# Kernel tuning notes

Hardware: AMD Instinct MI355X
Metric: run time of the kernel (lower is better)

Reference implementation:

```python
import jax, jax.numpy as jnp
import numpy as np

N = 100000    # nodes
E = 1600000   # edges (avg degree 16)
IN = 128      # input feature dim
D = 32        # per-head hidden dim
H = 4         # heads for hidden layers
C = 16        # num_classes (final per-head dim)
NEG = 0.2     # leaky_relu negative slope


def setup_inputs() -> dict:
    key = jax.random.key(0)
    ks = jax.random.split(key, 14)
    s = jnp.float32(0.05)
    f32 = jnp.float32
    inp = {
        "inputs": jax.random.normal(ks[0], (N, IN), f32),
        "src": jax.random.randint(ks[1], (E,), 0, N),
        "dst": jax.random.randint(ks[2], (E,), 0, N),
        # layer 0: IN -> (H, D), no residual
        "W0": jax.random.normal(ks[3], (IN, H * D), f32) * s,
        "al0": jax.random.normal(ks[4], (H, D), f32) * s,
        "ar0": jax.random.normal(ks[5], (H, D), f32) * s,
        # layer 1: H*D -> (H, D), identity residual (dims match)
        "W1": jax.random.normal(ks[6], (H * D, H * D), f32) * s,
        "al1": jax.random.normal(ks[7], (H, D), f32) * s,
        "ar1": jax.random.normal(ks[8], (H, D), f32) * s,
        # final layer: H*D -> (1, C), linear residual projection
        "W2": jax.random.normal(ks[9], (H * D, 1 * C), f32) * s,
        "al2": jax.random.normal(ks[10], (1, C), f32) * s,
        "ar2": jax.random.normal(ks[11], (1, C), f32) * s,
        "resW2": jax.random.normal(ks[12], (H * D, 1 * C), f32) * s,
    }
    return inp


def gat_conv(h, W, al, ar, src, dst, n_heads, out_dim, res=None, act=None):
    # h: (N, F_in) -> out: (N, n_heads, out_dim)
    feat = (h @ W).reshape(N, n_heads, out_dim)            # (N,H,D)
    el = jnp.sum(feat * al, axis=-1)                       # (N,H)
    er = jnp.sum(feat * ar, axis=-1)                       # (N,H)
    e = jax.nn.leaky_relu(el[src] + er[dst], NEG)          # (E,H)
    # softmax over incoming edges per destination node
    emax = jax.ops.segment_max(e, dst, num_segments=N)     # (N,H)
    ex = jnp.exp(e - emax[dst])                            # (E,H)
    den = jax.ops.segment_sum(ex, dst, num_segments=N)     # (N,H)
    alpha = ex / den[dst]                                  # (E,H)
    msg = feat[src] * alpha[:, :, None]                    # (E,H,D) -- dominant traffic
    out = jax.ops.segment_sum(msg, dst, num_segments=N)    # (N,H,D)
    if res is not None:
        out = out + res
    if act is not None:
        out = act(out)
    return out


def reference(inputs, src, dst, W0, al0, ar0, W1, al1, ar1, W2, al2, ar2, resW2):
    # hidden layer 0 (no residual), GATConv activation = elu, then flatten + relu
    h = gat_conv(inputs, W0, al0, ar0, src, dst, H, D, res=None, act=jax.nn.elu)
    h = jax.nn.relu(h.reshape(N, H * D))
    # hidden layer 1, identity residual (in == H*D)
    res1 = h.reshape(N, H, D)
    h = gat_conv(h, W1, al1, ar1, src, dst, H, D, res=res1, act=jax.nn.elu)
    h = jax.nn.relu(h.reshape(N, H * D))
    # output layer: 1 head, linear residual projection, no activation, mean over heads
    res2 = (h @ resW2).reshape(N, 1, C)
    out = gat_conv(h, W2, al2, ar2, src, dst, 1, C, res=res2, act=None)
    return out.mean(axis=1)                                # (N, C)
```

## Files before the change

kernel.cpp:

```cpp
#include <hip/hip_runtime.h>

#define N_NODES 100000
#define N_EDGES 1600000
#define IN_F    128
#define NEG_SLOPE 0.2f
#define NBUCK   512
#define PCHUNK  4096

typedef __attribute__((ext_vector_type(8))) short bf16x8;
typedef __attribute__((ext_vector_type(4))) float f32x4;

__device__ __forceinline__ float bf2f(unsigned short u) {
    return __uint_as_float(((unsigned int)u) << 16);
}

__device__ __forceinline__ unsigned short f2bf(float f) {
    unsigned int u = __float_as_uint(f);
    u += 0x7FFFu + ((u >> 16) & 1u);
    return (unsigned short)(u >> 16);
}

__global__ __launch_bounds__(256) void pack_all(const float* __restrict__ W0,
                                                const float* __restrict__ W1,
                                                const float* __restrict__ W2,
                                                const float* __restrict__ rW2,
                                                unsigned short* __restrict__ W0p,
                                                unsigned short* __restrict__ W1p,
                                                unsigned short* __restrict__ W2p) {
    int gid = blockIdx.x * 256 + threadIdx.x;
    const float* W;
    unsigned short* Wp;
    int idx, ncols;
    if (gid < 16384)      { W = W0; Wp = W0p; idx = gid;          ncols = 128; }
    else if (gid < 32768) { W = W1; Wp = W1p; idx = gid - 16384;  ncols = 128; }
    else                  { W = W2; Wp = W2p; idx = gid - 32768;  ncols = 32;  }
    int j  = idx & 7;
    int l  = (idx >> 3) & 63;
    int kt = (idx >> 9) & 3;
    int nt = idx >> 11;
    int k  = kt * 32 + (l >> 4) * 8 + j;
    int n  = nt * 16 + (l & 15);
    float v;
    if (ncols == 128) v = W[k * 128 + n];
    else              v = (n < 16) ? W[k * 16 + n] : rW2[k * 16 + (n - 16)];
    Wp[idx] = f2bf(v);
}

__global__ __launch_bounds__(256) void gemm128_mfma_f32(const float* __restrict__ A,
                                                        const unsigned short* __restrict__ Wp,
                                                        const float* __restrict__ al,
                                                        const float* __restrict__ ar,
                                                        unsigned short* __restrict__ featb,
                                                        float* __restrict__ el,
                                                        float* __restrict__ er,
                                                        int nrows) {
    const int t    = threadIdx.x;
    const int wv   = t >> 6;
    const int lane = t & 63;
    const int q    = lane >> 4;
    const int m    = lane & 15;
    const int rb   = blockIdx.x * 64 + wv * 16;
    const int arow = rb + m;
    const bool rok = arow < nrows;
    const float* Ar = A + (size_t)arow * IN_F;

    f32x4 acc[8];
#pragma unroll
    for (int nt = 0; nt < 8; ++nt) acc[nt] = (f32x4){0.f, 0.f, 0.f, 0.f};

#pragma unroll
    for (int kt = 0; kt < 4; ++kt) {
        bf16x8 afr = (bf16x8){0, 0, 0, 0, 0, 0, 0, 0};
        if (rok) {
            float4 v0 = *(const float4*)(Ar + kt * 32 + q * 8);
            float4 v1 = *(const float4*)(Ar + kt * 32 + q * 8 + 4);
            afr[0] = (short)f2bf(v0.x); afr[1] = (short)f2bf(v0.y);
            afr[2] = (short)f2bf(v0.z); afr[3] = (short)f2bf(v0.w);
            afr[4] = (short)f2bf(v1.x); afr[5] = (short)f2bf(v1.y);
            afr[6] = (short)f2bf(v1.z); afr[7] = (short)f2bf(v1.w);
        }
#pragma unroll
        for (int nt = 0; nt < 8; ++nt) {
            bf16x8 bfr = *(const bf16x8*)(Wp + ((size_t)(nt * 4 + kt) * 64 + lane) * 8);
            acc[nt] = __builtin_amdgcn_mfma_f32_16x16x32_bf16(afr, bfr, acc[nt], 0, 0, 0);
        }
    }

    float pel[16], per[16];
#pragma unroll
    for (int i = 0; i < 16; ++i) { pel[i] = 0.f; per[i] = 0.f; }

#pragma unroll
    for (int nt = 0; nt < 8; ++nt) {
        const int col = nt * 16 + m;
        const float alv = al[col];
        const float arv = ar[col];
        const int h = nt >> 1;
#pragma unroll
        for (int reg = 0; reg < 4; ++reg) {
            int row = rb + q * 4 + reg;
            float a = acc[nt][reg];
            if (row < nrows) featb[(size_t)row * 128 + col] = f2bf(a);
            pel[reg * 4 + h] += a * alv;
            per[reg * 4 + h] += a * arv;
        }
    }
#pragma unroll
    for (int s = 8; s > 0; s >>= 1) {
#pragma unroll
        for (int i = 0; i < 16; ++i) {
            pel[i] += __shfl_down(pel[i], s);
            per[i] += __shfl_down(per[i], s);
        }
    }
    if (m == 0) {
#pragma unroll
        for (int reg = 0; reg < 4; ++reg) {
            int row = rb + q * 4 + reg;
            if (row < nrows) {
#pragma unroll
                for (int h = 0; h < 4; ++h) {
                    el[row * 4 + h] = pel[reg * 4 + h];
                    er[row * 4 + h] = per[reg * 4 + h];
                }
            }
        }
    }
}

__global__ __launch_bounds__(256) void gemm128_mfma_bf16(const unsigned short* __restrict__ Ab,
                                                         const unsigned short* __restrict__ Wp,
                                                         const float* __restrict__ al,
                                                         const float* __restrict__ ar,
                                                         unsigned short* __restrict__ featb,
                                                         float* __restrict__ el,
                                                         float* __restrict__ er,
                                                         int nrows) {
    const int t    = threadIdx.x;
    const int wv   = t >> 6;
    const int lane = t & 63;
    const int q    = lane >> 4;
    const int m    = lane & 15;
    const int rb   = blockIdx.x * 64 + wv * 16;
    const int arow = rb + m;
    const bool rok = arow < nrows;
    const unsigned short* Ar = Ab + (size_t)arow * IN_F;

    f32x4 acc[8];
#pragma unroll
    for (int nt = 0; nt < 8; ++nt) acc[nt] = (f32x4){0.f, 0.f, 0.f, 0.f};

#pragma unroll
    for (int kt = 0; kt < 4; ++kt) {
        bf16x8 afr = (bf16x8){0, 0, 0, 0, 0, 0, 0, 0};
        if (rok) afr = *(const bf16x8*)(Ar + kt * 32 + q * 8);
#pragma unroll
        for (int nt = 0; nt < 8; ++nt) {
            bf16x8 bfr = *(const bf16x8*)(Wp + ((size_t)(nt * 4 + kt) * 64 + lane) * 8);
            acc[nt] = __builtin_amdgcn_mfma_f32_16x16x32_bf16(afr, bfr, acc[nt], 0, 0, 0);
        }
    }

    float pel[16], per[16];
#pragma unroll
    for (int i = 0; i < 16; ++i) { pel[i] = 0.f; per[i] = 0.f; }

#pragma unroll
    for (int nt = 0; nt < 8; ++nt) {
        const int col = nt * 16 + m;
        const float alv = al[col];
        const float arv = ar[col];
        const int h = nt >> 1;
#pragma unroll
        for (int reg = 0; reg < 4; ++reg) {
            int row = rb + q * 4 + reg;
            float a = acc[nt][reg];
            if (row < nrows) featb[(size_t)row * 128 + col] = f2bf(a);
            pel[reg * 4 + h] += a * alv;
            per[reg * 4 + h] += a * arv;
        }
    }
#pragma unroll
    for (int s = 8; s > 0; s >>= 1) {
#pragma unroll
        for (int i = 0; i < 16; ++i) {
            pel[i] += __shfl_down(pel[i], s);
            per[i] += __shfl_down(per[i], s);
        }
    }
    if (m == 0) {
#pragma unroll
        for (int reg = 0; reg < 4; ++reg) {
            int row = rb + q * 4 + reg;
            if (row < nrows) {
#pragma unroll
                for (int h = 0; h < 4; ++h) {
                    el[row * 4 + h] = pel[reg * 4 + h];
                    er[row * 4 + h] = per[reg * 4 + h];
                }
            }
        }
    }
}

__global__ __launch_bounds__(256) void gemm16_mfma(const unsigned short* __restrict__ Ab,
                                                   const unsigned short* __restrict__ Wp,
                                                   const float* __restrict__ al,
                                                   const float* __restrict__ ar,
                                                   unsigned short* __restrict__ feat2b,
                                                   float* __restrict__ res2,
                                                   float* __restrict__ el,
                                                   float* __restrict__ er,
                                                   int nrows) {
    const int t    = threadIdx.x;
    const int wv   = t >> 6;
    const int lane = t & 63;
    const int q    = lane >> 4;
    const int m    = lane & 15;
    const int rb   = blockIdx.x * 64 + wv * 16;
    const int arow = rb + m;
    const bool rok = arow < nrows;
    const unsigned short* Ar = Ab + (size_t)arow * IN_F;

    f32x4 acc0 = (f32x4){0.f, 0.f, 0.f, 0.f};
    f32x4 acc1 = (f32x4){0.f, 0.f, 0.f, 0.f};

#pragma unroll
    for (int kt = 0; kt < 4; ++kt) {
        bf16x8 afr = (bf16x8){0, 0, 0, 0, 0, 0, 0, 0};
        if (rok) afr = *(const bf16x8*)(Ar + kt * 32 + q * 8);
        bf16x8 b0 = *(const bf16x8*)(Wp + ((size_t)(0 * 4 + kt) * 64 + lane) * 8);
        bf16x8 b1 = *(const bf16x8*)(Wp + ((size_t)(1 * 4 + kt) * 64 + lane) * 8);
        acc0 = __builtin_amdgcn_mfma_f32_16x16x32_bf16(afr, b0, acc0, 0, 0, 0);
        acc1 = __builtin_amdgcn_mfma_f32_16x16x32_bf16(afr, b1, acc1, 0, 0, 0);
    }

    float pel[4], per[4];
    const float alv = al[m];
    const float arv = ar[m];
#pragma unroll
    for (int reg = 0; reg < 4; ++reg) {
        int row = rb + q * 4 + reg;
        float a = acc0[reg];
        if (row < nrows) {
            feat2b[(size_t)row * 16 + m] = f2bf(a);
            res2[(size_t)row * 16 + m]   = acc1[reg];
        }
        pel[reg] = a * alv;
        per[reg] = a * arv;
    }
#pragma unroll
    for (int s = 8; s > 0; s >>= 1) {
#pragma unroll
        for (int reg = 0; reg < 4; ++reg) {
            pel[reg] += __shfl_down(pel[reg], s);
            per[reg] += __shfl_down(per[reg], s);
        }
    }
    if (m == 0) {
#pragma unroll
        for (int reg = 0; reg < 4; ++reg) {
            int row = rb + q * 4 + reg;
            if (row < nrows) { el[row] = pel[reg]; er[row] = per[reg]; }
        }
    }
}

__global__ __launch_bounds__(256) void bucket_count_k(const int* __restrict__ dst,
                                                      int* __restrict__ bcount, int nE) {
    __shared__ int hist[NBUCK];
    const int t = threadIdx.x;
    hist[t] = 0; hist[t + 256] = 0;
    __syncthreads();
    const int start = blockIdx.x * PCHUNK;
#pragma unroll
    for (int j = 0; j < PCHUNK / 256; ++j) {
        int e = start + j * 256 + t;
        if (e < nE) atomicAdd(&hist[dst[e] >> 8], 1);
    }
    __syncthreads();
    if (hist[t])       atomicAdd(&bcount[t],       hist[t]);
    if (hist[t + 256]) atomicAdd(&bcount[t + 256], hist[t + 256]);
}

__global__ __launch_bounds__(NBUCK) void scan512(const int* __restrict__ bcount,
                                                 int* __restrict__ bbase,
                                                 int* __restrict__ bcursor) {
    __shared__ int s[NBUCK];
    const int t = threadIdx.x;
    int v = bcount[t];
    s[t] = v;
    __syncthreads();
#pragma unroll
    for (int off = 1; off < NBUCK; off <<= 1) {
        int x = (t >= off) ? s[t - off] : 0;
        __syncthreads();
        s[t] += x;
        __syncthreads();
    }
    int excl = s[t] - v;
    bbase[t]   = excl;
    bcursor[t] = excl;
}

__global__ __launch_bounds__(512) void partition_k(const int* __restrict__ src,
                                                   const int* __restrict__ dst,
                                                   int* __restrict__ bcursor,
                                                   unsigned int* __restrict__ pe, int nE) {
    __shared__ int hist[NBUCK];
    __shared__ int lstart[NBUCK];
    __shared__ int gbase[NBUCK];
    __shared__ int curB[NBUCK];
    __shared__ unsigned int reorder[PCHUNK];

    const int t = threadIdx.x;
    const int start = blockIdx.x * PCHUNK;
    const int m = min(PCHUNK, nE - start);

    hist[t] = 0;
    __syncthreads();

#pragma unroll
    for (int j = 0; j < PCHUNK / 512; ++j) {
        int e = start + j * 512 + t;
        if (e < nE) atomicAdd(&hist[dst[e] >> 8], 1);
    }
    __syncthreads();
    const int cnt = hist[t];

    __shared__ int s[NBUCK];
    s[t] = cnt;
    __syncthreads();
#pragma unroll
    for (int off = 1; off < NBUCK; off <<= 1) {
        int x = (t >= off) ? s[t - off] : 0;
        __syncthreads();
        s[t] += x;
        __syncthreads();
    }
    lstart[t] = s[t] - cnt;
    curB[t]   = s[t] - cnt;
    gbase[t] = cnt ? atomicAdd(&bcursor[t], cnt) : 0;
    __syncthreads();

#pragma unroll
    for (int j = 0; j < PCHUNK / 512; ++j) {
        int e = start + j * 512 + t;
        if (e < nE) {
            int d = dst[e];
            int pos = atomicAdd(&curB[d >> 8], 1);
            reorder[pos] = ((unsigned)src[e] << 8) | ((unsigned)d & 255u);
        }
    }
    __syncthreads();

    for (int i = t; i < m; i += 512) {
        unsigned int ed = reorder[i];
        int lo = 0, hi = NBUCK - 1;
        while (lo < hi) {
            int mid = (lo + hi + 1) >> 1;
            if (lstart[mid] <= i) lo = mid; else hi = mid - 1;
        }
        pe[gbase[lo] + (i - lstart[lo])] = ed;
    }
}

__global__ __launch_bounds__(256) void bucket_finalize(const unsigned int* __restrict__ pe,
                                                       const int* __restrict__ bbase,
                                                       int* __restrict__ rowptr,
                                                       int* __restrict__ deg,
                                                       int* __restrict__ sorted_src,
                                                       int nE) {
    __shared__ int deg_l[256];
    __shared__ int s[256];
    __shared__ int cur[256];

    const int b  = blockIdx.x;
    const int t  = threadIdx.x;
    const int base = bbase[b];
    const int endE = (b + 1 < NBUCK) ? bbase[b + 1] : nE;
    const int cnt  = endE - base;
    const int n    = b * 256 + t;

    deg_l[t] = 0;
    __syncthreads();
    for (int i = t; i < cnt; i += 256)
        atomicAdd(&deg_l[pe[base + i] & 255u], 1);
    __syncthreads();

    const int dv = deg_l[t];
    s[t] = dv;
    __syncthreads();
#pragma unroll
    for (int off = 1; off < 256; off <<= 1) {
        int x = (t >= off) ? s[t - off] : 0;
        __syncthreads();
        s[t] += x;
        __syncthreads();
    }
    const int off_l = s[t] - dv;
    if (n < N_NODES) {
        rowptr[n] = base + off_l;
        deg[n]    = dv;
    }
    cur[t] = off_l;
    __syncthreads();

    for (int i = t; i < cnt; i += 256) {
        unsigned int ed = pe[base + i];
        int pos = atomicAdd(&cur[ed & 255u], 1);
        sorted_src[base + pos] = (int)(ed >> 8);
    }
}

__global__ __launch_bounds__(256) void gat_agg128(const int* __restrict__ rowptr,
                                                  const int* __restrict__ deg,
                                                  const int* __restrict__ sorted_src,
                                                  const float* __restrict__ el,
                                                  const float* __restrict__ er,
                                                  const unsigned short* __restrict__ featb,
                                                  const unsigned short* __restrict__ resb,
                                                  unsigned short* __restrict__ outb) {
    __shared__ int   sS[4][64];
    __shared__ float sW[4][64][4];

    const int wv   = threadIdx.x >> 6;
    const int lane = threadIdx.x & 63;
    const int nd   = blockIdx.x * 4 + wv;

    const int dg = deg[nd];
    const int r0 = rowptr[nd];
    const int h  = lane >> 4;
    const float4 er4 = *(const float4*)(er + nd * 4);

    float den = 0.f;
    float ax = 0.f, ay = 0.f;

    for (int base = 0; base < dg; base += 64) {
        int m = dg - base; if (m > 64) m = 64;
        if (lane < m) {
            int s = sorted_src[r0 + base + lane];
            sS[wv][lane] = s;
            float4 e4 = *(const float4*)(el + s * 4);
            float4 w;
            float v;
            v = e4.x + er4.x; v = v > 0.f ? v : NEG_SLOPE * v; w.x = __expf(v);
            v = e4.y + er4.y; v = v > 0.f ? v : NEG_SLOPE * v; w.y = __expf(v);
            v = e4.z + er4.z; v = v > 0.f ? v : NEG_SLOPE * v; w.z = __expf(v);
            v = e4.w + er4.w; v = v > 0.f ? v : NEG_SLOPE * v; w.w = __expf(v);
            *(float4*)(&sW[wv][lane][0]) = w;
        }
        for (int i = 0; i < m; ++i) {
            int s   = sS[wv][i];
            float w = sW[wv][i][h];
            den += w;
            ushort2 u = *(const ushort2*)(featb + (size_t)s * 128 + lane * 2);
            ax += w * bf2f(u.x);
            ay += w * bf2f(u.y);
        }
    }

    float scale = den > 0.f ? 1.f / den : 0.f;
    float ox = ax * scale, oy = ay * scale;
    size_t o0 = (size_t)nd * 128 + lane * 2;
    if (resb) {
        ushort2 rv = *(const ushort2*)(resb + o0);
        ox += bf2f(rv.x);
        oy += bf2f(rv.y);
    }
    ox = fmaxf(ox, 0.f);
    oy = fmaxf(oy, 0.f);
    ushort2 ou;
    ou.x = f2bf(ox);
    ou.y = f2bf(oy);
    *(ushort2*)(outb + o0) = ou;
}

__global__ __launch_bounds__(256) void gat_agg16(const int* __restrict__ rowptr,
                                                 const int* __restrict__ deg,
                                                 const int* __restrict__ sorted_src,
                                                 const float* __restrict__ el,
                                                 const float* __restrict__ er,
                                                 const unsigned short* __restrict__ feat2b,
                                                 const float* __restrict__ res,
                                                 float* __restrict__ out) {
    __shared__ int   sS[4][64];
    __shared__ float sW[4][64];

    const int wv   = threadIdx.x >> 6;
    const int lane = threadIdx.x & 63;
    const int nd   = blockIdx.x * 4 + wv;
    const int g    = lane >> 3;
    const int f2   = (lane & 7) * 2;

    const int dg = deg[nd];
    const int r0 = rowptr[nd];
    const float erd = er[nd];

    float ax = 0.f, ay = 0.f, den = 0.f;

    for (int base = 0; base < dg; base += 64) {
        int m = dg - base; if (m > 64) m = 64;
        if (lane < m) {
            int s = sorted_src[r0 + base + lane];
            sS[wv][lane] = s;
            float v = el[s] + erd;
            v = v > 0.f ? v : NEG_SLOPE * v;
            sW[wv][lane] = __expf(v);
        }
        for (int i = g; i < m; i += 8) {
            int s   = sS[wv][i];
            float w = sW[wv][i];
            den += w;
            ushort2 u = *(const ushort2*)(feat2b + (size_t)s * 16 + f2);
            ax += w * bf2f(u.x);
            ay += w * bf2f(u.y);
        }
    }

    ax += __shfl_down(ax, 32); ay += __shfl_down(ay, 32); den += __shfl_down(den, 32);
    ax += __shfl_down(ax, 16); ay += __shfl_down(ay, 16); den += __shfl_down(den, 16);
    ax += __shfl_down(ax, 8);  ay += __shfl_down(ay, 8);  den += __shfl_down(den, 8);

    if (lane < 8) {
        float scale = den > 0.f ? 1.f / den : 0.f;
        size_t o0 = (size_t)nd * 16 + f2;
        float2 o;
        o.x = ax * scale + res[o0];
        o.y = ay * scale + res[o0 + 1];
        *(float2*)(out + o0) = o;
    }
}

extern "C" void kernel_launch(void* const* d_in, const int* in_sizes, int n_in,
                              void* d_out, int out_size, void* d_ws, size_t ws_size,
                              hipStream_t stream) {
    const float* inputs = (const float*)d_in[0];
    const int*   src    = (const int*)d_in[1];
    const int*   dst    = (const int*)d_in[2];
    const float* W0     = (const float*)d_in[3];
    const float* al0    = (const float*)d_in[4];
    const float* ar0    = (const float*)d_in[5];
    const float* W1     = (const float*)d_in[6];
    const float* al1    = (const float*)d_in[7];
    const float* ar1    = (const float*)d_in[8];
    const float* W2     = (const float*)d_in[9];
    const float* al2    = (const float*)d_in[10];
    const float* ar2    = (const float*)d_in[11];
    const float* resW2  = (const float*)d_in[12];
    float* out = (float*)d_out;

    const size_t NF = (size_t)N_NODES * 128;
    float* ws   = (float*)d_ws;
    float* el   = ws;
    float* er   = el + (size_t)N_NODES * 4;
    float* res2 = er + (size_t)N_NODES * 4;
    unsigned short* hbufb  = (unsigned short*)(res2 + (size_t)N_NODES * 16);
    unsigned short* featb  = hbufb + NF;
    unsigned short* feat2b = featb + NF;
    unsigned short* W0p    = feat2b + (size_t)N_NODES * 16;
    unsigned short* W1p    = W0p + 16384;
    unsigned short* W2p    = W1p + 16384;
    int* iws = (int*)(W2p + 8192);
    unsigned int* pe = (unsigned int*)iws;
    int* deg         = iws + N_EDGES;
    int* rowptr      = deg + N_NODES;
    int* sorted_src  = rowptr + N_NODES;
    int* bcount      = sorted_src + N_EDGES;
    int* bbase       = bcount + NBUCK;
    int* bcursor     = bbase + NBUCK;

    dim3 blk(256);
    int gemmGrid = (N_NODES + 63) / 64;
    int pGrid    = (N_EDGES + PCHUNK - 1) / PCHUNK;
    int bGrid    = (N_NODES + 255) / 256;
    int aggGrid  = N_NODES / 4;

    hipMemsetAsync(bcount, 0, NBUCK * sizeof(int), stream);
    bucket_count_k<<<pGrid, blk, 0, stream>>>(dst, bcount, N_EDGES);
    scan512<<<1, NBUCK, 0, stream>>>(bcount, bbase, bcursor);
    partition_k<<<pGrid, dim3(512), 0, stream>>>(src, dst, bcursor, pe, N_EDGES);
    bucket_finalize<<<bGrid, blk, 0, stream>>>(pe, bbase, rowptr, deg, sorted_src, N_EDGES);
    pack_all<<<160, blk, 0, stream>>>(W0, W1, W2, resW2, W0p, W1p, W2p);

    gemm128_mfma_f32<<<gemmGrid, blk, 0, stream>>>(inputs, W0p, al0, ar0, featb,
                                                   el, er, N_NODES);
    gat_agg128<<<aggGrid, blk, 0, stream>>>(rowptr, deg, sorted_src, el, er, featb,
                                            nullptr, hbufb);

    gemm128_mfma_bf16<<<gemmGrid, blk, 0, stream>>>(hbufb, W1p, al1, ar1, featb,
                                                    el, er, N_NODES);
    gat_agg128<<<aggGrid, blk, 0, stream>>>(rowptr, deg, sorted_src, el, er, featb,
                                            hbufb, hbufb);

    gemm16_mfma<<<gemmGrid, blk, 0, stream>>>(hbufb, W2p, al2, ar2, feat2b, res2,
                                              el, er, N_NODES);
    gat_agg16<<<aggGrid, blk, 0, stream>>>(rowptr, deg, sorted_src, el, er, feat2b,
                                           res2, out);
}
```

Before: 412.7 us.

## Horizontally fuse edge partitioning with layer-0 GEMM and bucket counting with weight packing

Merges the bucket-count kernel with weight packing, and the edge-partition kernel with the layer-0 feature GEMM, into single launches whose blocks branch on blockIdx. This cuts launch count and lets independent preprocessing and GEMM work overlap on the device. The partition step moves to 256 threads and records each slot's bucket in shared memory, replacing the per-element binary search. Nontemporal loads and stores are added on streaming accesses. The fused partition/GEMM kernel reserves about 34 KB of shared memory for every block, including GEMM blocks that do not use it, which may lower their occupancy.

```diff
diff --git a/kernel.cpp b/kernel.cpp
--- a/kernel.cpp
+++ b/kernel.cpp
@@ -6,9 +6,14 @@
 #define NEG_SLOPE 0.2f
 #define NBUCK   512
 #define PCHUNK  4096
+#define PGRID   391
+#define GEMMGRID 1563
+#define PACKGRID 160
 
 typedef __attribute__((ext_vector_type(8))) short bf16x8;
 typedef __attribute__((ext_vector_type(4))) float f32x4;
+typedef __attribute__((ext_vector_type(2))) float f32x2;
+typedef __attribute__((ext_vector_type(2))) unsigned short u16x2;
 
 __device__ __forceinline__ float bf2f(unsigned short u) {
     return __uint_as_float(((unsigned int)u) << 16);
@@ -20,111 +25,263 @@
     return (unsigned short)(u >> 16);
 }
 
-__global__ __launch_bounds__(256) void pack_all(const float* __restrict__ W0,
-                                                const float* __restrict__ W1,
-                                                const float* __restrict__ W2,
-                                                const float* __restrict__ rW2,
-                                                unsigned short* __restrict__ W0p,
-                                                unsigned short* __restrict__ W1p,
-                                                unsigned short* __restrict__ W2p) {
-    int gid = blockIdx.x * 256 + threadIdx.x;
-    const float* W;
-    unsigned short* Wp;
-    int idx, ncols;
-    if (gid < 16384)      { W = W0; Wp = W0p; idx = gid;          ncols = 128; }
-    else if (gid < 32768) { W = W1; Wp = W1p; idx = gid - 16384;  ncols = 128; }
-    else                  { W = W2; Wp = W2p; idx = gid - 32768;  ncols = 32;  }
-    int j  = idx & 7;
-    int l  = (idx >> 3) & 63;
-    int kt = (idx >> 9) & 3;
-    int nt = idx >> 11;
-    int k  = kt * 32 + (l >> 4) * 8 + j;
-    int n  = nt * 16 + (l & 15);
-    float v;
-    if (ncols == 128) v = W[k * 128 + n];
-    else              v = (n < 16) ? W[k * 16 + n] : rW2[k * 16 + (n - 16)];
-    Wp[idx] = f2bf(v);
-}
-
-__global__ __launch_bounds__(256) void gemm128_mfma_f32(const float* __restrict__ A,
-                                                        const unsigned short* __restrict__ Wp,
-                                                        const float* __restrict__ al,
-                                                        const float* __restrict__ ar,
-                                                        unsigned short* __restrict__ featb,
-                                                        float* __restrict__ el,
-                                                        float* __restrict__ er,
-                                                        int nrows) {
-    const int t    = threadIdx.x;
-    const int wv   = t >> 6;
-    const int lane = t & 63;
-    const int q    = lane >> 4;
-    const int m    = lane & 15;
-    const int rb   = blockIdx.x * 64 + wv * 16;
-    const int arow = rb + m;
-    const bool rok = arow < nrows;
-    const float* Ar = A + (size_t)arow * IN_F;
-
-    f32x4 acc[8];
-#pragma unroll
-    for (int nt = 0; nt < 8; ++nt) acc[nt] = (f32x4){0.f, 0.f, 0.f, 0.f};
-
-#pragma unroll
-    for (int kt = 0; kt < 4; ++kt) {
-        bf16x8 afr = (bf16x8){0, 0, 0, 0, 0, 0, 0, 0};
-        if (rok) {
-            float4 v0 = *(const float4*)(Ar + kt * 32 + q * 8);
-            float4 v1 = *(const float4*)(Ar + kt * 32 + q * 8 + 4);
-            afr[0] = (short)f2bf(v0.x); afr[1] = (short)f2bf(v0.y);
-            afr[2] = (short)f2bf(v0.z); afr[3] = (short)f2bf(v0.w);
-            afr[4] = (short)f2bf(v1.x); afr[5] = (short)f2bf(v1.y);
-            afr[6] = (short)f2bf(v1.z); afr[7] = (short)f2bf(v1.w);
-        }
+__global__ __launch_bounds__(256) void count_pack(const int* __restrict__ dst,
+                                                  int* __restrict__ bcount, int nE,
+                                                  const float* __restrict__ W0,
+                                                  const float* __restrict__ W1,
+                                                  const float* __restrict__ W2,
+                                                  const float* __restrict__ rW2,
+                                                  unsigned short* __restrict__ W0p,
+                                                  unsigned short* __restrict__ W1p,
+                                                  unsigned short* __restrict__ W2p) {
+    __shared__ int hist[NBUCK];
+    const int t = threadIdx.x;
+    if (blockIdx.x < PGRID) {
+        hist[t] = 0; hist[t + 256] = 0;
+        __syncthreads();
+        const int start = blockIdx.x * PCHUNK;
+#pragma unroll
+        for (int j = 0; j < PCHUNK / 256; ++j) {
+            int e = start + j * 256 + t;
+            if (e < nE) atomicAdd(&hist[__builtin_nontemporal_load(dst + e) >> 8], 1);
+        }
+        __syncthreads();
+        if (hist[t])       atomicAdd(&bcount[t],       hist[t]);
+        if (hist[t + 256]) atomicAdd(&bcount[t + 256], hist[t + 256]);
+    } else {
+        int gid = (blockIdx.x - PGRID) * 256 + t;
+        const float* W;
+        unsigned short* Wp;
+        int idx, ncols;
+        if (gid < 16384)      { W = W0; Wp = W0p; idx = gid;          ncols = 128; }
+        else if (gid < 32768) { W = W1; Wp = W1p; idx = gid - 16384;  ncols = 128; }
+        else                  { W = W2; Wp = W2p; idx = gid - 32768;  ncols = 32;  }
+        int j  = idx & 7;
+        int l  = (idx >> 3) & 63;
+        int kt = (idx >> 9) & 3;
+        int nt = idx >> 11;
+        int k  = kt * 32 + (l >> 4) * 8 + j;
+        int n  = nt * 16 + (l & 15);
+        float v;
+        if (ncols == 128) v = W[k * 128 + n];
+        else              v = (n < 16) ? W[k * 16 + n] : rW2[k * 16 + (n - 16)];
+        Wp[idx] = f2bf(v);
+    }
+}
+
+__global__ __launch_bounds__(NBUCK) void scan512(const int* __restrict__ bcount,
+                                                 int* __restrict__ bbase,
+                                                 int* __restrict__ bcursor) {
+    __shared__ int s[NBUCK];
+    const int t = threadIdx.x;
+    int v = bcount[t];
+    s[t] = v;
+    __syncthreads();
+#pragma unroll
+    for (int off = 1; off < NBUCK; off <<= 1) {
+        int x = (t >= off) ? s[t - off] : 0;
+        __syncthreads();
+        s[t] += x;
+        __syncthreads();
+    }
+    int excl = s[t] - v;
+    bbase[t]   = excl;
+    bcursor[t] = excl;
+}
+
+__global__ __launch_bounds__(256) void part_gemm0(const int* __restrict__ src,
+                                                  const int* __restrict__ dst,
+                                                  int* __restrict__ bcursor,
+                                                  unsigned int* __restrict__ pe, int nE,
+                                                  const float* __restrict__ A,
+                                                  const unsigned short* __restrict__ Wp,
+                                                  const float* __restrict__ al,
+                                                  const float* __restrict__ ar,
+                                                  unsigned short* __restrict__ featb,
+                                                  float* __restrict__ el,
+                                                  float* __restrict__ er,
+                                                  int nrows) {
+    __shared__ int hist[NBUCK];
+    __shared__ int lstart[NBUCK];
+    __shared__ int gbase[NBUCK];
+    __shared__ int curB[NBUCK];
+    __shared__ int s[NBUCK];
+    __shared__ unsigned int  reorder[PCHUNK];
+    __shared__ unsigned short bmem[PCHUNK];
+
+    const int t = threadIdx.x;
+
+    if (blockIdx.x < PGRID) {
+        const int start = blockIdx.x * PCHUNK;
+        const int m = min(PCHUNK, nE - start);
+
+        hist[t] = 0; hist[t + 256] = 0;
+        __syncthreads();
+#pragma unroll
+        for (int j = 0; j < PCHUNK / 256; ++j) {
+            int e = start + j * 256 + t;
+            if (e < nE) atomicAdd(&hist[__builtin_nontemporal_load(dst + e) >> 8], 1);
+        }
+        __syncthreads();
+        const int c0 = hist[t];
+        const int c1 = hist[t + 256];
+        s[t] = c0; s[t + 256] = c1;
+        __syncthreads();
+#pragma unroll
+        for (int off = 1; off <= 256; off <<= 1) {
+            int x0 = (t >= off) ? s[t - off] : 0;
+            int x1 = s[t + 256 - off];
+            __syncthreads();
+            s[t] += x0; s[t + 256] += x1;
+            __syncthreads();
+        }
+        lstart[t]       = s[t] - c0;
+        lstart[t + 256] = s[t + 256] - c1;
+        curB[t]         = s[t] - c0;
+        curB[t + 256]   = s[t + 256] - c1;
+        gbase[t]        = c0 ? atomicAdd(&bcursor[t],       c0) : 0;
+        gbase[t + 256]  = c1 ? atomicAdd(&bcursor[t + 256], c1) : 0;
+        __syncthreads();
+
+#pragma unroll
+        for (int j = 0; j < PCHUNK / 256; ++j) {
+            int e = start + j * 256 + t;
+            if (e < nE) {
+                int d  = __builtin_nontemporal_load(dst + e);
+                int sv = __builtin_nontemporal_load(src + e);
+                int b  = d >> 8;
+                int pos = atomicAdd(&curB[b], 1);
+                reorder[pos] = ((unsigned)sv << 8) | ((unsigned)d & 255u);
+                bmem[pos]    = (unsigned short)b;
+            }
+        }
+        __syncthreads();
+
+        for (int i = t; i < m; i += 256) {
+            int b = bmem[i];
+            __builtin_nontemporal_store(reorder[i], pe + gbase[b] + (i - lstart[b]));
+        }
+    } else {
+        const int bid  = blockIdx.x - PGRID;
+        const int wv   = t >> 6;
+        const int lane = t & 63;
+        const int q    = lane >> 4;
+        const int m    = lane & 15;
+        const int rb   = bid * 64 + wv * 16;
+        const int arow = rb + m;
+        const bool rok = arow < nrows;
+        const float* Ar = A + (size_t)arow * IN_F;
+
+        f32x4 acc[8];
+#pragma unroll
+        for (int nt = 0; nt < 8; ++nt) acc[nt] = (f32x4){0.f, 0.f, 0.f, 0.f};
+
+#pragma unroll
+        for (int kt = 0; kt < 4; ++kt) {
+            bf16x8 afr = (bf16x8){0, 0, 0, 0, 0, 0, 0, 0};
+            if (rok) {
+                f32x4 v0 = __builtin_nontemporal_load((const f32x4*)(Ar + kt * 32 + q * 8));
+                f32x4 v1 = __builtin_nontemporal_load((const f32x4*)(Ar + kt * 32 + q * 8 + 4));
+                afr[0] = (short)f2bf(v0.x); afr[1] = (short)f2bf(v0.y);
+                afr[2] = (short)f2bf(v0.z); afr[3] = (short)f2bf(v0.w);
+                afr[4] = (short)f2bf(v1.x); afr[5] = (short)f2bf(v1.y);
+                afr[6] = (short)f2bf(v1.z); afr[7] = (short)f2bf(v1.w);
+            }
+#pragma unroll
+            for (int nt = 0; nt < 8; ++nt) {
+                bf16x8 bfr = *(const bf16x8*)(Wp + ((size_t)(nt * 4 + kt) * 64 + lane) * 8);
+                acc[nt] = __builtin_amdgcn_mfma_f32_16x16x32_bf16(afr, bfr, acc[nt], 0, 0, 0);
+            }
+        }
+
+        float pel[16], per[16];
+#pragma unroll
+        for (int i = 0; i < 16; ++i) { pel[i] = 0.f; per[i] = 0.f; }
+
 #pragma unroll
         for (int nt = 0; nt < 8; ++nt) {
-            bf16x8 bfr = *(const bf16x8*)(Wp + ((size_t)(nt * 4 + kt) * 64 + lane) * 8);
-            acc[nt] = __builtin_amdgcn_mfma_f32_16x16x32_bf16(afr, bfr, acc[nt], 0, 0, 0);
-        }
-    }
-
-    float pel[16], per[16];
-#pragma unroll
-    for (int i = 0; i < 16; ++i) { pel[i] = 0.f; per[i] = 0.f; }
-
-#pragma unroll
-    for (int nt = 0; nt < 8; ++nt) {
-        const int col = nt * 16 + m;
-        const float alv = al[col];
-        const float arv = ar[col];
-        const int h = nt >> 1;
-#pragma unroll
-        for (int reg = 0; reg < 4; ++reg) {
-            int row = rb + q * 4 + reg;
-            float a = acc[nt][reg];
-            if (row < nrows) featb[(size_t)row * 128 + col] = f2bf(a);
-            pel[reg * 4 + h] += a * alv;
-            per[reg * 4 + h] += a * arv;
-        }
-    }
-#pragma unroll
-    for (int s = 8; s > 0; s >>= 1) {
-#pragma unroll
-        for (int i = 0; i < 16; ++i) {
-            pel[i] += __shfl_down(pel[i], s);
-            per[i] += __shfl_down(per[i], s);
-        }
-    }
-    if (m == 0) {
-#pragma unroll
-        for (int reg = 0; reg < 4; ++reg) {
-            int row = rb + q * 4 + reg;
-            if (row < nrows) {
-#pragma unroll
-                for (int h = 0; h < 4; ++h) {
-                    el[row * 4 + h] = pel[reg * 4 + h];
-                    er[row * 4 + h] = per[reg * 4 + h];
+            const int col = nt * 16 + m;
+            const float alv = al[col];
+            const float arv = ar[col];
+            const int h = nt >> 1;
+#pragma unroll
+            for (int reg = 0; reg < 4; ++reg) {
+                int row = rb + q * 4 + reg;
+                float a = acc[nt][reg];
+                if (row < nrows) featb[(size_t)row * 128 + col] = f2bf(a);
+                pel[reg * 4 + h] += a * alv;
+                per[reg * 4 + h] += a * arv;
+            }
+        }
+#pragma unroll
+        for (int sh = 8; sh > 0; sh >>= 1) {
+#pragma unroll
+            for (int i = 0; i < 16; ++i) {
+                pel[i] += __shfl_down(pel[i], sh);
+                per[i] += __shfl_down(per[i], sh);
+            }
+        }
+        if (m == 0) {
+#pragma unroll
+            for (int reg = 0; reg < 4; ++reg) {
+                int row = rb + q * 4 + reg;
+                if (row < nrows) {
+#pragma unroll
+                    for (int h = 0; h < 4; ++h) {
+                        el[row * 4 + h] = pel[reg * 4 + h];
+                        er[row * 4 + h] = per[reg * 4 + h];
+                    }
                 }
             }
         }
+    }
+}
+
+__global__ __launch_bounds__(256) void bucket_finalize(const unsigned int* __restrict__ pe,
+                                                       const int* __restrict__ bbase,
+                                                       int* __restrict__ rowptr,
+                                                       int* __restrict__ deg,
+                                                       int* __restrict__ sorted_src,
+                                                       int nE) {
+    __shared__ int deg_l[256];
+    __shared__ int s[256];
+    __shared__ int cur[256];
+
+    const int b  = blockIdx.x;
+    const int t  = threadIdx.x;
+    const int base = bbase[b];
+    const int endE = (b + 1 < NBUCK) ? bbase[b + 1] : nE;
+    const int cnt  = endE - base;
+    const int n    = b * 256 + t;
+
+    deg_l[t] = 0;
+    __syncthreads();
+    for (int i = t; i < cnt; i += 256)
+        atomicAdd(&deg_l[__builtin_nontemporal_load(pe + base + i) & 255u], 1);
+    __syncthreads();
+
+    const int dv = deg_l[t];
+    s[t] = dv;
+    __syncthreads();
+#pragma unroll
+    for (int off = 1; off < 256; off <<= 1) {
+        int x = (t >= off) ? s[t - off] : 0;
+        __syncthreads();
+        s[t] += x;
+        __syncthreads();
+    }
+    const int off_l = s[t] - dv;
+    if (n < N_NODES) {
+        rowptr[n] = base + off_l;
+        deg[n]    = dv;
+    }
+    cur[t] = off_l;
+    __syncthreads();
+
+    for (int i = t; i < cnt; i += 256) {
+        unsigned int ed = __builtin_nontemporal_load(pe + base + i);
+        int pos = atomicAdd(&cur[ed & 255u], 1);
+        sorted_src[base + pos] = (int)(ed >> 8);
     }
 }
 
@@ -153,7 +310,7 @@
 #pragma unroll
     for (int kt = 0; kt < 4; ++kt) {
         bf16x8 afr = (bf16x8){0, 0, 0, 0, 0, 0, 0, 0};
-        if (rok) afr = *(const bf16x8*)(Ar + kt * 32 + q * 8);
+        if (rok) afr = __builtin_nontemporal_load((const bf16x8*)(Ar + kt * 32 + q * 8));
 #pragma unroll
         for (int nt = 0; nt < 8; ++nt) {
             bf16x8 bfr = *(const bf16x8*)(Wp + ((size_t)(nt * 4 + kt) * 64 + lane) * 8);
@@ -181,11 +338,11 @@
         }
     }
 #pragma unroll
-    for (int s = 8; s > 0; s >>= 1) {
+    for (int sh = 8; sh > 0; sh >>= 1) {
 #pragma unroll
         for (int i = 0; i < 16; ++i) {
-            pel[i] += __shfl_down(pel[i], s);
-            per[i] += __shfl_down(per[i], s);
+            pel[i] += __shfl_down(pel[i], sh);
+            per[i] += __shfl_down(per[i], sh);
         }
     }
     if (m == 0) {
@@ -228,7 +385,7 @@
 #pragma unroll
     for (int kt = 0; kt < 4; ++kt) {
         bf16x8 afr = (bf16x8){0, 0, 0, 0, 0, 0, 0, 0};
-        if (rok) afr = *(const bf16x8*)(Ar + kt * 32 + q * 8);
+        if (rok) afr = __builtin_nontemporal_load((const bf16x8*)(Ar + kt * 32 + q * 8));
         bf16x8 b0 = *(const bf16x8*)(Wp + ((size_t)(0 * 4 + kt) * 64 + lane) * 8);
         bf16x8 b1 = *(const bf16x8*)(Wp + ((size_t)(1 * 4 + kt) * 64 + lane) * 8);
         acc0 = __builtin_amdgcn_mfma_f32_16x16x32_bf16(afr, b0, acc0, 0, 0, 0);
@@ -244,17 +401,17 @@
         float a = acc0[reg];
         if (row < nrows) {
             feat2b[(size_t)row * 16 + m] = f2bf(a);
-            res2[(size_t)row * 16 + m]   = acc1[reg];
+            __builtin_nontemporal_store(acc1[reg], res2 + (size_t)row * 16 + m);
         }
         pel[reg] = a * alv;
         per[reg] = a * arv;
     }
 #pragma unroll
-    for (int s = 8; s > 0; s >>= 1) {
+    for (int sh = 8; sh > 0; sh >>= 1) {
 #pragma unroll
         for (int reg = 0; reg < 4; ++reg) {
-            pel[reg] += __shfl_down(pel[reg], s);
-            per[reg] += __shfl_down(per[reg], s);
+            pel[reg] += __shfl_down(pel[reg], sh);
+            per[reg] += __shfl_down(per[reg], sh);
         }
     }
     if (m == 0) {
@@ -263,153 +420,6 @@
             int row = rb + q * 4 + reg;
             if (row < nrows) { el[row] = pel[reg]; er[row] = per[reg]; }
         }
-    }
-}
-
-__global__ __launch_bounds__(256) void bucket_count_k(const int* __restrict__ dst,
-                                                      int* __restrict__ bcount, int nE) {
-    __shared__ int hist[NBUCK];
-    const int t = threadIdx.x;
-    hist[t] = 0; hist[t + 256] = 0;
-    __syncthreads();
-    const int start = blockIdx.x * PCHUNK;
-#pragma unroll
-    for (int j = 0; j < PCHUNK / 256; ++j) {
-        int e = start + j * 256 + t;
-        if (e < nE) atomicAdd(&hist[dst[e] >> 8], 1);
-    }
-    __syncthreads();
-    if (hist[t])       atomicAdd(&bcount[t],       hist[t]);
-    if (hist[t + 256]) atomicAdd(&bcount[t + 256], hist[t + 256]);
-}
-
-__global__ __launch_bounds__(NBUCK) void scan512(const int* __restrict__ bcount,
-                                                 int* __restrict__ bbase,
-                                                 int* __restrict__ bcursor) {
-    __shared__ int s[NBUCK];
-    const int t = threadIdx.x;
-    int v = bcount[t];
-    s[t] = v;
-    __syncthreads();
-#pragma unroll
-    for (int off = 1; off < NBUCK; off <<= 1) {
-        int x = (t >= off) ? s[t - off] : 0;
-        __syncthreads();
-        s[t] += x;
-        __syncthreads();
-    }
-    int excl = s[t] - v;
-    bbase[t]   = excl;
-    bcursor[t] = excl;
-}
-
-__global__ __launch_bounds__(512) void partition_k(const int* __restrict__ src,
-                                                   const int* __restrict__ dst,
-                                                   int* __restrict__ bcursor,
-                                                   unsigned int* __restrict__ pe, int nE) {
-    __shared__ int hist[NBUCK];
-    __shared__ int lstart[NBUCK];
-    __shared__ int gbase[NBUCK];
-    __shared__ int curB[NBUCK];
-    __shared__ unsigned int reorder[PCHUNK];
-
-    const int t = threadIdx.x;
-    const int start = blockIdx.x * PCHUNK;
-    const int m = min(PCHUNK, nE - start);
-
-    hist[t] = 0;
-    __syncthreads();
-
-#pragma unroll
-    for (int j = 0; j < PCHUNK / 512; ++j) {
-        int e = start + j * 512 + t;
-        if (e < nE) atomicAdd(&hist[dst[e] >> 8], 1);
-    }
-    __syncthreads();
-    const int cnt = hist[t];
-
-    __shared__ int s[NBUCK];
-    s[t] = cnt;
-    __syncthreads();
-#pragma unroll
-    for (int off = 1; off < NBUCK; off <<= 1) {
-        int x = (t >= off) ? s[t - off] : 0;
-        __syncthreads();
-        s[t] += x;
-        __syncthreads();
-    }
-    lstart[t] = s[t] - cnt;
-    curB[t]   = s[t] - cnt;
-    gbase[t] = cnt ? atomicAdd(&bcursor[t], cnt) : 0;
-    __syncthreads();
-
-#pragma unroll
-    for (int j = 0; j < PCHUNK / 512; ++j) {
-        int e = start + j * 512 + t;
-        if (e < nE) {
-            int d = dst[e];
-            int pos = atomicAdd(&curB[d >> 8], 1);
-            reorder[pos] = ((unsigned)src[e] << 8) | ((unsigned)d & 255u);
-        }
-    }
-    __syncthreads();
-
-    for (int i = t; i < m; i += 512) {
-        unsigned int ed = reorder[i];
-        int lo = 0, hi = NBUCK - 1;
-        while (lo < hi) {
-            int mid = (lo + hi + 1) >> 1;
-            if (lstart[mid] <= i) lo = mid; else hi = mid - 1;
-        }
-        pe[gbase[lo] + (i - lstart[lo])] = ed;
-    }
-}
-
-__global__ __launch_bounds__(256) void bucket_finalize(const unsigned int* __restrict__ pe,
-                                                       const int* __restrict__ bbase,
-                                                       int* __restrict__ rowptr,
-                                                       int* __restrict__ deg,
-                                                       int* __restrict__ sorted_src,
-                                                       int nE) {
-    __shared__ int deg_l[256];
-    __shared__ int s[256];
-    __shared__ int cur[256];
-
-    const int b  = blockIdx.x;
-    const int t  = threadIdx.x;
-    const int base = bbase[b];
-    const int endE = (b + 1 < NBUCK) ? bbase[b + 1] : nE;
-    const int cnt  = endE - base;
-    const int n    = b * 256 + t;
-
-    deg_l[t] = 0;
-    __syncthreads();
-    for (int i = t; i < cnt; i += 256)
-        atomicAdd(&deg_l[pe[base + i] & 255u], 1);
-    __syncthreads();
-
-    const int dv = deg_l[t];
-    s[t] = dv;
-    __syncthreads();
-#pragma unroll
-    for (int off = 1; off < 256; off <<= 1) {
-        int x = (t >= off) ? s[t - off] : 0;
-        __syncthreads();
-        s[t] += x;
-        __syncthreads();
-    }
-    const int off_l = s[t] - dv;
-    if (n < N_NODES) {
-        rowptr[n] = base + off_l;
-        deg[n]    = dv;
-    }
-    cur[t] = off_l;
-    __syncthreads();
-
-    for (int i = t; i < cnt; i += 256) {
-        unsigned int ed = pe[base + i];
-        int pos = atomicAdd(&cur[ed & 255u], 1);
-        sorted_src[base + pos] = (int)(ed >> 8);
     }
 }
 
@@ -439,7 +449,7 @@
     for (int base = 0; base < dg; base += 64) {
         int m = dg - base; if (m > 64) m = 64;
         if (lane < m) {
-            int s = sorted_src[r0 + base + lane];
+            int s = __builtin_nontemporal_load(sorted_src + r0 + base + lane);
             sS[wv][lane] = s;
             float4 e4 = *(const float4*)(el + s * 4);
             float4 w;
@@ -454,7 +464,7 @@
             int s   = sS[wv][i];
             float w = sW[wv][i][h];
             den += w;
-            ushort2 u = *(const ushort2*)(featb + (size_t)s * 128 + lane * 2);
+            u16x2 u = *((const u16x2*)(featb + (size_t)s * 128) + lane);
             ax += w * bf2f(u.x);
             ay += w * bf2f(u.y);
         }
@@ -464,16 +474,16 @@
     float ox = ax * scale, oy = ay * scale;
     size_t o0 = (size_t)nd * 128 + lane * 2;
     if (resb) {
-        ushort2 rv = *(const ushort2*)(resb + o0);
+        u16x2 rv = __builtin_nontemporal_load((const u16x2*)(resb + o0));
         ox += bf2f(rv.x);
         oy += bf2f(rv.y);
     }
     ox = fmaxf(ox, 0.f);
     oy = fmaxf(oy, 0.f);
-    ushort2 ou;
+    u16x2 ou;
     ou.x = f2bf(ox);
     ou.y = f2bf(oy);
-    *(ushort2*)(outb + o0) = ou;
+    __builtin_nontemporal_store(ou, (u16x2*)(outb + o0));
 }
 
 __global__ __launch_bounds__(256) void gat_agg16(const int* __restrict__ rowptr,
@@ -502,7 +512,7 @@
     for (int base = 0; base < dg; base += 64) {
         int m = dg - base; if (m > 64) m = 64;
         if (lane < m) {
-            int s = sorted_src[r0 + base + lane];
+            int s = __builtin_nontemporal_load(sorted_src + r0 + base + lane);
             sS[wv][lane] = s;
             float v = el[s] + erd;
             v = v > 0.f ? v : NEG_SLOPE * v;
@@ -512,7 +522,7 @@
             int s   = sS[wv][i];
             float w = sW[wv][i];
             den += w;
-            ushort2 u = *(const ushort2*)(feat2b + (size_t)s * 16 + f2);
+            u16x2 u = *(const u16x2*)(feat2b + (size_t)s * 16 + f2);
             ax += w * bf2f(u.x);
             ay += w * bf2f(u.y);
         }
@@ -525,10 +535,10 @@
     if (lane < 8) {
         float scale = den > 0.f ? 1.f / den : 0.f;
         size_t o0 = (size_t)nd * 16 + f2;
-        float2 o;
-        o.x = ax * scale + res[o0];
-        o.y = ay * scale + res[o0 + 1];
-        *(float2*)(out + o0) = o;
+        f32x2 o;
+        o.x = ax * scale + __builtin_nontemporal_load(res + o0);
+        o.y = ay * scale + __builtin_nontemporal_load(res + o0 + 1);
+        __builtin_nontemporal_store(o, (f32x2*)(out + o0));
     }
 }
 
@@ -571,29 +581,27 @@
     int* bcursor     = bbase + NBUCK;
 
     dim3 blk(256);
-    int gemmGrid = (N_NODES + 63) / 64;
-    int pGrid    = (N_EDGES + PCHUNK - 1) / PCHUNK;
-    int bGrid    = (N_NODES + 255) / 256;
-    int aggGrid  = N_NODES / 4;
+    int bGrid   = (N_NODES + 255) / 256;
+    int aggGrid = N_NODES / 4;
 
     hipMemsetAsync(bcount, 0, NBUCK * sizeof(int), stream);
-    bucket_count_k<<<pGrid, blk, 0, stream>>>(dst, bcount, N_EDGES);
+    count_pack<<<PGRID + PACKGRID, blk, 0, stream>>>(dst, bcount, N_EDGES,
+                                                     W0, W1, W2, resW2, W0p, W1p, W2p);
     scan512<<<1, NBUCK, 0, stream>>>(bcount, bbase, bcursor);
-    partition_k<<<pGrid, dim3(512), 0, stream>>>(src, dst, bcursor, pe, N_EDGES);
+    part_gemm0<<<PGRID + GEMMGRID, blk, 0, stream>>>(src, dst, bcursor, pe, N_EDGES,
+                                                     inputs, W0p, al0, ar0, featb,
+                                                     el, er, N_NODES);
     bucket_finalize<<<bGrid, blk, 0, stream>>>(pe, bbase, rowptr, deg, sorted_src, N_EDGES);
-    pack_all<<<160, blk, 0, stream>>>(W0, W1, W2, resW2, W0p, W1p, W2p);
-
-    gemm128_mfma_f32<<<gemmGrid, blk, 0, stream>>>(inputs, W0p, al0, ar0, featb,
-                                                   el, er, N_NODES);
+
     gat_agg128<<<aggGrid, blk, 0, stream>>>(rowptr, deg, sorted_src, el, er, featb,
                                             nullptr, hbufb);
 
-    gemm128_mfma_bf16<<<gemmGrid, blk, 0, stream>>>(hbufb, W1p, al1, ar1, featb,
+    gemm128_mfma_bf16<<<GEMMGRID, blk, 0, stream>>>(hbufb, W1p, al1, ar1, featb,
                                                     el, er, N_NODES);
     gat_agg128<<<aggGrid, blk, 0, stream>>>(rowptr, deg, sorted_src, el, er, featb,
                                             hbufb, hbufb);
 
-    gemm16_mfma<<<gemmGrid, blk, 0, stream>>>(hbufb, W2p, al2, ar2, feat2b, res2,
+    gemm16_mfma<<<GEMMGRID, blk, 0, stream>>>(hbufb, W2p, al2, ar2, feat2b, res2,
                                               el, er, N_NODES);
     gat_agg16<<<aggGrid, blk, 0, stream>>>(rowptr, deg, sorted_src, el, er, feat2b,
                                            res2, out);
```

Measured after the change: 423.6 us. 2.6% more time.
